# Performance work log

Measured on AMD Instinct MI355X. Metric: run time of the kernel, lower is better.

Reference implementation:

```python
import jax, jax.numpy as jnp
import numpy as np

B, L, HID, NH = 2, 2048, 1024, 16
HD = HID // NH  # 64


def setup_inputs() -> dict:
    key = jax.random.key(0)
    ks = jax.random.split(key, 12)
    s = 1.0 / np.sqrt(HID)
    query = jax.random.normal(ks[0], (B, L, HID), jnp.float32)
    key_t = jax.random.normal(ks[1], (B, L, HID), jnp.float32)
    value = jax.random.normal(ks[2], (B, L, HID), jnp.float32)
    # key padding mask: True = valid token; random lengths in [1024, 2048]
    lengths = jax.random.randint(ks[3], (B,), L // 2, L + 1)
    key_mask = jnp.arange(L)[None, :] < lengths[:, None]  # [B, K] bool
    # attn_mask: True = blocked (causal upper triangle), 2D branch [Q, K]
    attn_mask = jnp.triu(jnp.ones((L, L), jnp.bool_), k=1)
    Wq = jax.random.normal(ks[4], (HID, HID), jnp.float32) * s
    Wk = jax.random.normal(ks[5], (HID, HID), jnp.float32) * s
    Wv = jax.random.normal(ks[6], (HID, HID), jnp.float32) * s
    Wo = jax.random.normal(ks[7], (HID, HID), jnp.float32) * s
    bq = jax.random.normal(ks[8], (HID,), jnp.float32) * 0.01
    bk = jax.random.normal(ks[9], (HID,), jnp.float32) * 0.01
    bv = jax.random.normal(ks[10], (HID,), jnp.float32) * 0.01
    bo = jax.random.normal(ks[11], (HID,), jnp.float32) * 0.01
    return {"query": query, "key": key_t, "value": value,
            "key_mask": key_mask, "attn_mask": attn_mask,
            "Wq": Wq, "bq": bq, "Wk": Wk, "bk": bk,
            "Wv": Wv, "bv": bv, "Wo": Wo, "bo": bo}


def reference(query, key, value, key_mask, attn_mask,
              Wq, bq, Wk, bk, Wv, bv, Wo, bo):
    Bq, Q, _ = query.shape
    K = key.shape[1]
    # projections (torch Linear: x @ W.T + b), split heads -> [B, H, L, HD]
    def proj(x, W, b, L_):
        return (x @ W.T + b).reshape(Bq, L_, NH, HD).transpose(0, 2, 1, 3)
    q = proj(query, Wq, bq, Q)
    k = proj(key, Wk, bk, K)
    v = proj(value, Wv, bv, K)
    scores = jnp.einsum('bhqd,bhkd->bhqk', q, k) / np.sqrt(HD)
    blocked = attn_mask[None, None, :, :]                 # True = blocked
    kmask = key_mask[:, None, None, :]                    # True = valid
    valid = (~blocked) & kmask                            # [B,H,Q,K] (bcast)
    scores = jnp.where(blocked, -10000.0, scores)
    scores = jnp.where(kmask, scores, -10000.0)
    weights = jax.nn.softmax(scores, axis=-1)
    weights = weights * valid.astype(weights.dtype)
    weights = weights / jnp.maximum(weights.sum(-1, keepdims=True), 1e-6)
    attended = jnp.einsum('bhqk,bhkd->bhqd', weights, v)
    attended = attended.transpose(0, 2, 1, 3).reshape(Bq, Q, HID)
    return attended @ Wo.T + bo
```

## Files before the change

kernel.cpp:

```cpp
#include <hip/hip_runtime.h>
#include <hip/hip_bf16.h>
#include <stdint.h>


#define L_SEQ 2048
#define HID 1024
#define NHEAD 16
#define HD 64

typedef __attribute__((ext_vector_type(8))) short bf16x8;
typedef __attribute__((ext_vector_type(8))) unsigned short u16x8;
typedef __attribute__((ext_vector_type(4))) float f32x4;

__device__ __forceinline__ unsigned short f2bf(float f) {
  unsigned int u = __builtin_bit_cast(unsigned int, f);
  u += 0x7fffu + ((u >> 16) & 1u);
  return (unsigned short)(u >> 16);
}

__device__ __forceinline__ unsigned int pk2bf(float a, float b) {
  unsigned int r;
  asm("v_cvt_pk_bf16_f32 %0, %1, %2" : "=v"(r) : "v"(a), "v"(b));
  return r;
}

__device__ __forceinline__ void gl_lds16(const void* g, void* l) {
  __builtin_amdgcn_global_load_lds(
      (const __attribute__((address_space(1))) unsigned int*)(uintptr_t)g,
      (__attribute__((address_space(3))) unsigned int*)(uint32_t)(uintptr_t)l,
      16, 0, 0);
}

__device__ __forceinline__ f32x4 mfma16(bf16x8 a, bf16x8 b, f32x4 c) {
  return __builtin_amdgcn_mfma_f32_16x16x32_bf16(a, b, c, 0, 0, 0);
}

__global__ __launch_bounds__(256)
void convert_all_kernel(const float* __restrict__ q, const float* __restrict__ k,
                        const float* __restrict__ v, const float* __restrict__ wq,
                        const float* __restrict__ wk, const float* __restrict__ wv,
                        const float* __restrict__ wo, const unsigned int* __restrict__ km,
                        unsigned short* __restrict__ qb, unsigned short* __restrict__ kb,
                        unsigned short* __restrict__ vb, unsigned short* __restrict__ wqb,
                        unsigned short* __restrict__ wkb, unsigned short* __restrict__ wvb,
                        unsigned short* __restrict__ wob, int* __restrict__ lens) {
  __shared__ int red[256];
  const int bid = blockIdx.x;
  const int t = threadIdx.x;
  if (bid == 8192) {
    unsigned int w0 = km[0];
    bool u8mode = (w0 != 1u);
    for (int b = 0; b < 2; ++b) {
      int cnt = 0;
      if (u8mode) {
        const unsigned char* p = (const unsigned char*)km + b * L_SEQ;
        for (int i = t; i < L_SEQ; i += 256) cnt += (p[i] != 0) ? 1 : 0;
      } else {
        const unsigned int* p = km + b * L_SEQ;
        for (int i = t; i < L_SEQ; i += 256) cnt += (p[i] != 0) ? 1 : 0;
      }
      red[t] = cnt;
      __syncthreads();
      for (int s = 128; s > 0; s >>= 1) {
        if (t < s) red[t] += red[t + s];
        __syncthreads();
      }
      if (t == 0) lens[b] = red[0];
      __syncthreads();
    }
    return;
  }
  const float* src;
  unsigned short* dst;
  int base;
  if (bid < 6144) {
    int s = bid >> 11;
    base = (bid & 2047) * 2048;
    src = s == 0 ? q : (s == 1 ? k : v);
    dst = s == 0 ? qb : (s == 1 ? kb : vb);
  } else {
    int r = bid - 6144;
    int s = r >> 9;
    base = (r & 511) * 2048;
    src = s == 0 ? wq : (s == 1 ? wk : (s == 2 ? wv : wo));
    dst = s == 0 ? wqb : (s == 1 ? wkb : (s == 2 ? wvb : wob));
  }
  int i = base + t * 8;
  float4 a = *(const float4*)(src + i);
  float4 b4 = *(const float4*)(src + i + 4);
  u16x8 o;
  o[0] = f2bf(a.x); o[1] = f2bf(a.y); o[2] = f2bf(a.z); o[3] = f2bf(a.w);
  o[4] = f2bf(b4.x); o[5] = f2bf(b4.y); o[6] = f2bf(b4.z); o[7] = f2bf(b4.w);
  *(u16x8*)(dst + i) = o;
}

__device__ __forceinline__ void gemm128_core(const unsigned short* __restrict__ A,
                                             const unsigned short* __restrict__ W,
                                             int m0, int n0, int K,
                                             unsigned short* As, unsigned short* Bs,
                                             f32x4 acc[4][4]) {
  const int tid = threadIdx.x;
  const int w = tid >> 6, lane = tid & 63;
  const int l15 = lane & 15, l4 = lane >> 4;
  const int wr = w >> 1, wc = w & 1;
#pragma unroll
  for (int i = 0; i < 4; ++i)
#pragma unroll
    for (int j = 0; j < 4; ++j) acc[i][j] = (f32x4){0.f, 0.f, 0.f, 0.f};

  for (int k0 = 0; k0 < K; k0 += 32) {
#pragma unroll
    for (int i = 0; i < 2; ++i) {
      int c = i * 256 + tid;
      int row = c >> 2, col = (c & 3) * 8;
      gl_lds16(A + (size_t)(m0 + row) * K + k0 + col, (char*)As + (i * 256 + w * 64) * 16);
      gl_lds16(W + (size_t)(n0 + row) * K + k0 + col, (char*)Bs + (i * 256 + w * 64) * 16);
    }
    __syncthreads();
    bf16x8 af[4], bfr[4];
#pragma unroll
    for (int i = 0; i < 4; ++i)
      af[i] = *(const bf16x8*)(As + (wr * 64 + i * 16 + l15) * 32 + l4 * 8);
#pragma unroll
    for (int j = 0; j < 4; ++j)
      bfr[j] = *(const bf16x8*)(Bs + (wc * 64 + j * 16 + l15) * 32 + l4 * 8);
    __builtin_amdgcn_s_setprio(1);
#pragma unroll
    for (int i = 0; i < 4; ++i)
#pragma unroll
      for (int j = 0; j < 4; ++j) acc[i][j] = mfma16(af[i], bfr[j], acc[i][j]);
    __builtin_amdgcn_s_setprio(0);
    __syncthreads();
  }
}

__global__ __launch_bounds__(256)
void qkv_gemm_kernel(const unsigned short* __restrict__ qb, const unsigned short* __restrict__ kb,
                     const unsigned short* __restrict__ vb, const unsigned short* __restrict__ wq,
                     const unsigned short* __restrict__ wk, const unsigned short* __restrict__ wv,
                     const float* __restrict__ bq, const float* __restrict__ bk,
                     const float* __restrict__ bv, unsigned short* __restrict__ Qp,
                     unsigned short* __restrict__ Kp, unsigned short* __restrict__ Vtp) {
  __shared__ unsigned short As[128 * 32];
  __shared__ unsigned short Bs[128 * 32];
  const int z = blockIdx.z;
  const unsigned short* A = z == 0 ? qb : (z == 1 ? kb : vb);
  const unsigned short* W = z == 0 ? wq : (z == 1 ? wk : wv);
  const float* bias = z == 0 ? bq : (z == 1 ? bk : bv);
  const int m0 = blockIdx.y * 128, n0 = blockIdx.x * 128;
  f32x4 acc[4][4];
  gemm128_core(A, W, m0, n0, HID, As, Bs, acc);

  const int tid = threadIdx.x;
  const int w = tid >> 6, lane = tid & 63;
  const int l15 = lane & 15, l4 = lane >> 4;
  const int wr = w >> 1, wc = w & 1;
  const float scale = (z == 0) ? 0.125f * 1.44269504089f : 1.0f;
#pragma unroll
  for (int i = 0; i < 4; ++i)
#pragma unroll
    for (int j = 0; j < 4; ++j)
#pragma unroll
      for (int r = 0; r < 4; ++r) {
        int grow = m0 + wr * 64 + i * 16 + l4 * 4 + r;
        int gcol = n0 + wc * 64 + j * 16 + l15;
        float v = (acc[i][j][r] + bias[gcol]) * scale;
        int bb = grow >> 11, ll = grow & 2047;
        int hh = gcol >> 6, d = gcol & 63;
        unsigned short o = f2bf(v);
        if (z == 0)
          Qp[((size_t)(bb * NHEAD + hh) * L_SEQ + ll) * HD + d] = o;
        else if (z == 1)
          Kp[((size_t)(bb * NHEAD + hh) * L_SEQ + ll) * HD + d] = o;
        else
          Vtp[((size_t)(bb * NHEAD + hh) * HD + d) * L_SEQ + ll] = o;
      }
}

__global__ __launch_bounds__(256)
void out_gemm_kernel(const unsigned short* __restrict__ att, const unsigned short* __restrict__ wo,
                     const float* __restrict__ bo, float* __restrict__ out) {
  __shared__ unsigned short As[128 * 32];
  __shared__ unsigned short Bs[128 * 32];
  const int m0 = blockIdx.y * 128, n0 = blockIdx.x * 128;
  f32x4 acc[4][4];
  gemm128_core(att, wo, m0, n0, HID, As, Bs, acc);

  const int tid = threadIdx.x;
  const int w = tid >> 6, lane = tid & 63;
  const int l15 = lane & 15, l4 = lane >> 4;
  const int wr = w >> 1, wc = w & 1;
#pragma unroll
  for (int i = 0; i < 4; ++i)
#pragma unroll
    for (int j = 0; j < 4; ++j)
#pragma unroll
      for (int r = 0; r < 4; ++r) {
        int grow = m0 + wr * 64 + i * 16 + l4 * 4 + r;
        int gcol = n0 + wc * 64 + j * 16 + l15;
        out[(size_t)grow * HID + gcol] = acc[i][j][r] + bo[gcol];
      }
}

__global__ __launch_bounds__(512)
void attn_kernel(const unsigned short* __restrict__ Qp, const unsigned short* __restrict__ Kp,
                 const unsigned short* __restrict__ Vtp, unsigned short* __restrict__ att,
                 const int* __restrict__ lens) {
  __shared__ unsigned short Ks[2][64 * 64];
  __shared__ unsigned short Vs[2][64 * 64];
  __shared__ unsigned short Ps[8][16 * 72];

  const int x = blockIdx.x, bh = blockIdx.y;
  const int b = bh >> 4, h = bh & 15;
  const int tid = threadIdx.x, w = tid >> 6, lane = tid & 63;
  const int l15 = lane & 15, l4 = lane >> 4;
  const int len = lens[b];
  const int sub = (w < 4) ? x : (31 - x);
  const int qw0 = sub * 64 + (w & 3) * 16;

  const unsigned short* Qg = Qp + (size_t)bh * L_SEQ * HD;
  const unsigned short* Kg = Kp + (size_t)bh * L_SEQ * HD;
  const unsigned short* Vg = Vtp + (size_t)bh * HD * L_SEQ;

  const int rr = tid >> 3, cb = tid & 7;
  const int swz = (cb ^ (rr & 7)) * 8;
  const unsigned short* KgRow = Kg + (size_t)rr * HD + swz;
  const unsigned short* VgRow = Vg + (size_t)rr * L_SEQ + swz;

  bf16x8 qf[2];
#pragma unroll
  for (int kk = 0; kk < 2; ++kk)
    qf[kk] = *(const bf16x8*)(Qg + (size_t)(qw0 + l15) * HD + kk * 32 + l4 * 8);

  f32x4 acc[4];
#pragma unroll
  for (int n = 0; n < 4; ++n) acc[n] = (f32x4){0.f, 0.f, 0.f, 0.f};
  float mq = -1e30f, lq = 0.f;

  int koff[4][2];
#pragma unroll
  for (int n = 0; n < 4; ++n)
#pragma unroll
    for (int kk = 0; kk < 2; ++kk) {
      int row = n * 16 + l15;
      koff[n][kk] = row * 128 + (((l4 + kk * 4) ^ (row & 7)) * 16);
    }

  const int len_r = ((len + 63) >> 6) << 6;
  const int hi_end = 64 * (32 - x);
  const int kv_end = (hi_end < len_r) ? hi_end : len_r;
  const int nt = kv_end >> 6;

  gl_lds16(KgRow, (char*)&Ks[0][0] + w * 1024);
  gl_lds16(VgRow, (char*)&Vs[0][0] + w * 1024);
  __syncthreads();

  int cur = 0;
  for (int t = 0; t < nt; ++t) {
    const int k0 = t * 64;
    if (t + 1 < nt) {
      const int k1 = k0 + 64;
      gl_lds16(KgRow + (size_t)k1 * HD, (char*)&Ks[cur ^ 1][0] + w * 1024);
      gl_lds16(VgRow + k1, (char*)&Vs[cur ^ 1][0] + w * 1024);
    }
    if (k0 <= qw0 + 15) {
      const char* Kb = (const char*)&Ks[cur][0];
      const char* Vb = (const char*)&Vs[cur][0];
      f32x4 s[4];
#pragma unroll
      for (int n = 0; n < 4; ++n) s[n] = (f32x4){0.f, 0.f, 0.f, 0.f};
      __builtin_amdgcn_s_setprio(1);
#pragma unroll
      for (int kk = 0; kk < 2; ++kk) {
#pragma unroll
        for (int n = 0; n < 4; ++n)
          s[n] = mfma16(*(const bf16x8*)(Kb + koff[n][kk]), qf[kk], s[n]);
      }
      __builtin_amdgcn_s_setprio(0);
      if (!(k0 + 63 <= qw0 && k0 + 64 <= len)) {
        const int qa = qw0 + l15;
#pragma unroll
        for (int n = 0; n < 4; ++n)
#pragma unroll
          for (int r = 0; r < 4; ++r) {
            int ka = k0 + n * 16 + l4 * 4 + r;
            if (ka > qa || ka >= len) s[n][r] = -1e30f;
          }
      }
      float v01 = fmaxf(fmaxf(s[0][0], s[0][1]), fmaxf(s[0][2], s[0][3]));
      float v23 = fmaxf(fmaxf(s[1][0], s[1][1]), fmaxf(s[1][2], s[1][3]));
      float v45 = fmaxf(fmaxf(s[2][0], s[2][1]), fmaxf(s[2][2], s[2][3]));
      float v67 = fmaxf(fmaxf(s[3][0], s[3][1]), fmaxf(s[3][2], s[3][3]));
      float v = fmaxf(fmaxf(v01, v23), fmaxf(v45, v67));
      v = fmaxf(v, __shfl_xor(v, 16));
      v = fmaxf(v, __shfl_xor(v, 32));
      float mold = mq;
      float mnew = fmaxf(mold, v);
      mq = mnew;
      float alpha = __builtin_amdgcn_exp2f(mold - mnew);
      float rs = 0.f;
#pragma unroll
      for (int n = 0; n < 4; ++n)
#pragma unroll
        for (int r = 0; r < 4; ++r) {
          float p = __builtin_amdgcn_exp2f(s[n][r] - mnew);
          s[n][r] = p;
          rs += p;
        }
      rs += __shfl_xor(rs, 16);
      rs += __shfl_xor(rs, 32);
      lq = lq * alpha + rs;
      float ar[4];
#pragma unroll
      for (int r = 0; r < 4; ++r) ar[r] = __shfl(alpha, l4 * 4 + r, 64);
#pragma unroll
      for (int n = 0; n < 4; ++n)
#pragma unroll
        for (int r = 0; r < 4; ++r) acc[n][r] *= ar[r];
#pragma unroll
      for (int n = 0; n < 4; ++n) {
        uint2 pw;
        pw.x = pk2bf(s[n][0], s[n][1]);
        pw.y = pk2bf(s[n][2], s[n][3]);
        *(uint2*)(&Ps[w][l15 * 72 + n * 16 + l4 * 4]) = pw;
      }
      bf16x8 pf[2];
#pragma unroll
      for (int kk = 0; kk < 2; ++kk)
        pf[kk] = *(const bf16x8*)(&Ps[w][l15 * 72 + kk * 32 + l4 * 8]);
      __builtin_amdgcn_s_setprio(1);
#pragma unroll
      for (int kk = 0; kk < 2; ++kk) {
#pragma unroll
        for (int n = 0; n < 4; ++n)
          acc[n] = mfma16(pf[kk], *(const bf16x8*)(Vb + koff[n][kk]), acc[n]);
      }
      __builtin_amdgcn_s_setprio(0);
    }
    __syncthreads();
    cur ^= 1;
  }

  float invq = 1.0f / lq;
  float invr[4];
#pragma unroll
  for (int r = 0; r < 4; ++r) invr[r] = __shfl(invq, l4 * 4 + r, 64);
#pragma unroll
  for (int r = 0; r < 4; ++r) {
    int qa = qw0 + l4 * 4 + r;
#pragma unroll
    for (int n = 0; n < 4; ++n)
      att[((size_t)(b * L_SEQ + qa)) * HID + h * HD + n * 16 + l15] = f2bf(acc[n][r] * invr[r]);
  }
}

extern "C" void kernel_launch(void* const* d_in, const int* in_sizes, int n_in,
                              void* d_out, int out_size, void* d_ws, size_t ws_size,
                              hipStream_t stream) {
  const float* query = (const float*)d_in[0];
  const float* key = (const float*)d_in[1];
  const float* value = (const float*)d_in[2];
  const unsigned int* key_mask = (const unsigned int*)d_in[3];
  const float* Wq = (const float*)d_in[5];
  const float* bq = (const float*)d_in[6];
  const float* Wk = (const float*)d_in[7];
  const float* bk = (const float*)d_in[8];
  const float* Wv = (const float*)d_in[9];
  const float* bv = (const float*)d_in[10];
  const float* Wo = (const float*)d_in[11];
  const float* bo = (const float*)d_in[12];

  char* ws = (char*)d_ws;
  const size_t SZ_X = (size_t)4096 * 1024 * 2;
  const size_t SZ_W = (size_t)1024 * 1024 * 2;
  unsigned short* qb = (unsigned short*)(ws);
  unsigned short* kb = (unsigned short*)(ws + SZ_X);
  unsigned short* vb = (unsigned short*)(ws + 2 * SZ_X);
  unsigned short* wqb = (unsigned short*)(ws + 3 * SZ_X);
  unsigned short* wkb = (unsigned short*)(ws + 3 * SZ_X + SZ_W);
  unsigned short* wvb = (unsigned short*)(ws + 3 * SZ_X + 2 * SZ_W);
  unsigned short* wob = (unsigned short*)(ws + 3 * SZ_X + 3 * SZ_W);
  unsigned short* Qp = (unsigned short*)(ws + 3 * SZ_X + 4 * SZ_W);
  unsigned short* Kp = (unsigned short*)(ws + 4 * SZ_X + 4 * SZ_W);
  unsigned short* Vtp = (unsigned short*)(ws + 5 * SZ_X + 4 * SZ_W);
  unsigned short* att = (unsigned short*)(ws + 6 * SZ_X + 4 * SZ_W);
  int* lens = (int*)(ws + 7 * SZ_X + 4 * SZ_W);

  convert_all_kernel<<<8193, 256, 0, stream>>>(query, key, value, Wq, Wk, Wv, Wo, key_mask,
                                               qb, kb, vb, wqb, wkb, wvb, wob, lens);
  qkv_gemm_kernel<<<dim3(8, 32, 3), 256, 0, stream>>>(qb, kb, vb, wqb, wkb, wvb, bq, bk, bv,
                                                      Qp, Kp, Vtp);
  attn_kernel<<<dim3(16, 32), 512, 0, stream>>>(Qp, Kp, Vtp, att, lens);
  out_gemm_kernel<<<dim3(8, 32), 256, 0, stream>>>(att, wob, bo, (float*)d_out);
}
```

Baseline: 146.8 us.

## Double-buffer GEMM LDS tiles, vectorize V-transpose stores, lazy softmax rescale

The shared 128x128 GEMM core now double-buffers its LDS tiles, so the next K-slice's global-to-LDS load is issued before the current slice's MFMAs and one barrier per iteration is removed. The QKV epilogue for V writes four consecutive sequence positions as one packed 8-byte store into the transposed layout instead of scalar 2-byte stores. The attention kernel skips the running-max update and accumulator rescale unless some lane's new max exceeds the old one by more than 8 (in log2 units). This lets unnormalized probabilities grow up to 2^8 before rescaling, and it doubles LDS use per GEMM block, which may lower occupancy.

New measurement: 129.7 us. 11.6% less time.

```diff
diff --git a/kernel.cpp b/kernel.cpp
--- a/kernel.cpp
+++ b/kernel.cpp
@@ -94,11 +94,11 @@
   *(u16x8*)(dst + i) = o;
 }
 
-__device__ __forceinline__ void gemm128_core(const unsigned short* __restrict__ A,
-                                             const unsigned short* __restrict__ W,
-                                             int m0, int n0, int K,
-                                             unsigned short* As, unsigned short* Bs,
-                                             f32x4 acc[4][4]) {
+__device__ __forceinline__ void gemm128_bf_core(const unsigned short* __restrict__ A,
+                                                const unsigned short* __restrict__ W,
+                                                int m0, int n0, int K,
+                                                unsigned short* As, unsigned short* Bs,
+                                                f32x4 acc[4][4]) {
   const int tid = threadIdx.x;
   const int w = tid >> 6, lane = tid & 63;
   const int l15 = lane & 15, l4 = lane >> 4;
@@ -108,22 +108,39 @@
 #pragma unroll
     for (int j = 0; j < 4; ++j) acc[i][j] = (f32x4){0.f, 0.f, 0.f, 0.f};
 
-  for (int k0 = 0; k0 < K; k0 += 32) {
-#pragma unroll
-    for (int i = 0; i < 2; ++i) {
-      int c = i * 256 + tid;
-      int row = c >> 2, col = (c & 3) * 8;
-      gl_lds16(A + (size_t)(m0 + row) * K + k0 + col, (char*)As + (i * 256 + w * 64) * 16);
-      gl_lds16(W + (size_t)(n0 + row) * K + k0 + col, (char*)Bs + (i * 256 + w * 64) * 16);
+  const int nk = K >> 5;
+#pragma unroll
+  for (int i = 0; i < 2; ++i) {
+    int c = i * 256 + tid;
+    int row = c >> 2, col = (c & 3) * 8;
+    gl_lds16(A + (size_t)(m0 + row) * K + col, (char*)As + (i * 256 + w * 64) * 16);
+    gl_lds16(W + (size_t)(n0 + row) * K + col, (char*)Bs + (i * 256 + w * 64) * 16);
+  }
+  __syncthreads();
+
+  int cur = 0;
+  for (int t = 0; t < nk; ++t) {
+    const int k0 = t * 32;
+    if (t + 1 < nk) {
+#pragma unroll
+      for (int i = 0; i < 2; ++i) {
+        int c = i * 256 + tid;
+        int row = c >> 2, col = (c & 3) * 8;
+        gl_lds16(A + (size_t)(m0 + row) * K + k0 + 32 + col,
+                 (char*)As + (cur ^ 1) * 8192 + (i * 256 + w * 64) * 16);
+        gl_lds16(W + (size_t)(n0 + row) * K + k0 + 32 + col,
+                 (char*)Bs + (cur ^ 1) * 8192 + (i * 256 + w * 64) * 16);
+      }
     }
-    __syncthreads();
+    const unsigned short* Asb = As + cur * 4096;
+    const unsigned short* Bsb = Bs + cur * 4096;
     bf16x8 af[4], bfr[4];
 #pragma unroll
     for (int i = 0; i < 4; ++i)
-      af[i] = *(const bf16x8*)(As + (wr * 64 + i * 16 + l15) * 32 + l4 * 8);
+      af[i] = *(const bf16x8*)(Asb + (wr * 64 + i * 16 + l15) * 32 + l4 * 8);
 #pragma unroll
     for (int j = 0; j < 4; ++j)
-      bfr[j] = *(const bf16x8*)(Bs + (wc * 64 + j * 16 + l15) * 32 + l4 * 8);
+      bfr[j] = *(const bf16x8*)(Bsb + (wc * 64 + j * 16 + l15) * 32 + l4 * 8);
     __builtin_amdgcn_s_setprio(1);
 #pragma unroll
     for (int i = 0; i < 4; ++i)
@@ -131,6 +148,7 @@
       for (int j = 0; j < 4; ++j) acc[i][j] = mfma16(af[i], bfr[j], acc[i][j]);
     __builtin_amdgcn_s_setprio(0);
     __syncthreads();
+    cur ^= 1;
   }
 }
 
@@ -141,50 +159,62 @@
                      const float* __restrict__ bq, const float* __restrict__ bk,
                      const float* __restrict__ bv, unsigned short* __restrict__ Qp,
                      unsigned short* __restrict__ Kp, unsigned short* __restrict__ Vtp) {
-  __shared__ unsigned short As[128 * 32];
-  __shared__ unsigned short Bs[128 * 32];
+  __shared__ unsigned short As[2 * 128 * 32];
+  __shared__ unsigned short Bs[2 * 128 * 32];
   const int z = blockIdx.z;
   const unsigned short* A = z == 0 ? qb : (z == 1 ? kb : vb);
   const unsigned short* W = z == 0 ? wq : (z == 1 ? wk : wv);
   const float* bias = z == 0 ? bq : (z == 1 ? bk : bv);
   const int m0 = blockIdx.y * 128, n0 = blockIdx.x * 128;
   f32x4 acc[4][4];
-  gemm128_core(A, W, m0, n0, HID, As, Bs, acc);
+  gemm128_bf_core(A, W, m0, n0, HID, As, Bs, acc);
 
   const int tid = threadIdx.x;
   const int w = tid >> 6, lane = tid & 63;
   const int l15 = lane & 15, l4 = lane >> 4;
   const int wr = w >> 1, wc = w & 1;
   const float scale = (z == 0) ? 0.125f * 1.44269504089f : 1.0f;
-#pragma unroll
-  for (int i = 0; i < 4; ++i)
-#pragma unroll
-    for (int j = 0; j < 4; ++j)
-#pragma unroll
-      for (int r = 0; r < 4; ++r) {
-        int grow = m0 + wr * 64 + i * 16 + l4 * 4 + r;
+  if (z == 2) {
+#pragma unroll
+    for (int i = 0; i < 4; ++i)
+#pragma unroll
+      for (int j = 0; j < 4; ++j) {
+        int grow0 = m0 + wr * 64 + i * 16 + l4 * 4;
         int gcol = n0 + wc * 64 + j * 16 + l15;
-        float v = (acc[i][j][r] + bias[gcol]) * scale;
-        int bb = grow >> 11, ll = grow & 2047;
+        float bv_ = bias[gcol];
+        int bb = grow0 >> 11, ll0 = grow0 & 2047;
         int hh = gcol >> 6, d = gcol & 63;
-        unsigned short o = f2bf(v);
-        if (z == 0)
-          Qp[((size_t)(bb * NHEAD + hh) * L_SEQ + ll) * HD + d] = o;
-        else if (z == 1)
-          Kp[((size_t)(bb * NHEAD + hh) * L_SEQ + ll) * HD + d] = o;
-        else
-          Vtp[((size_t)(bb * NHEAD + hh) * HD + d) * L_SEQ + ll] = o;
-      }
+        uint2 pw;
+        pw.x = pk2bf(acc[i][j][0] + bv_, acc[i][j][1] + bv_);
+        pw.y = pk2bf(acc[i][j][2] + bv_, acc[i][j][3] + bv_);
+        *(uint2*)(&Vtp[((size_t)(bb * NHEAD + hh) * HD + d) * L_SEQ + ll0]) = pw;
+      }
+  } else {
+    unsigned short* P = (z == 0) ? Qp : Kp;
+#pragma unroll
+    for (int i = 0; i < 4; ++i)
+#pragma unroll
+      for (int j = 0; j < 4; ++j)
+#pragma unroll
+        for (int r = 0; r < 4; ++r) {
+          int grow = m0 + wr * 64 + i * 16 + l4 * 4 + r;
+          int gcol = n0 + wc * 64 + j * 16 + l15;
+          float v = (acc[i][j][r] + bias[gcol]) * scale;
+          int bb = grow >> 11, ll = grow & 2047;
+          int hh = gcol >> 6, d = gcol & 63;
+          P[((size_t)(bb * NHEAD + hh) * L_SEQ + ll) * HD + d] = f2bf(v);
+        }
+  }
 }
 
 __global__ __launch_bounds__(256)
 void out_gemm_kernel(const unsigned short* __restrict__ att, const unsigned short* __restrict__ wo,
                      const float* __restrict__ bo, float* __restrict__ out) {
-  __shared__ unsigned short As[128 * 32];
-  __shared__ unsigned short Bs[128 * 32];
+  __shared__ unsigned short As[2 * 128 * 32];
+  __shared__ unsigned short Bs[2 * 128 * 32];
   const int m0 = blockIdx.y * 128, n0 = blockIdx.x * 128;
   f32x4 acc[4][4];
-  gemm128_core(att, wo, m0, n0, HID, As, Bs, acc);
+  gemm128_bf_core(att, wo, m0, n0, HID, As, Bs, acc);
 
   const int tid = threadIdx.x;
   const int w = tid >> 6, lane = tid & 63;
@@ -294,29 +324,31 @@
       float v = fmaxf(fmaxf(v01, v23), fmaxf(v45, v67));
       v = fmaxf(v, __shfl_xor(v, 16));
       v = fmaxf(v, __shfl_xor(v, 32));
-      float mold = mq;
-      float mnew = fmaxf(mold, v);
-      mq = mnew;
-      float alpha = __builtin_amdgcn_exp2f(mold - mnew);
+      if (!__all(v - mq <= 8.0f)) {
+        float mnew = fmaxf(mq, v);
+        float alpha = __builtin_amdgcn_exp2f(mq - mnew);
+        mq = mnew;
+        float ar[4];
+#pragma unroll
+        for (int r = 0; r < 4; ++r) ar[r] = __shfl(alpha, l4 * 4 + r, 64);
+#pragma unroll
+        for (int n = 0; n < 4; ++n)
+#pragma unroll
+          for (int r = 0; r < 4; ++r) acc[n][r] *= ar[r];
+        lq *= alpha;
+      }
       float rs = 0.f;
 #pragma unroll
       for (int n = 0; n < 4; ++n)
 #pragma unroll
         for (int r = 0; r < 4; ++r) {
-          float p = __builtin_amdgcn_exp2f(s[n][r] - mnew);
+          float p = __builtin_amdgcn_exp2f(s[n][r] - mq);
           s[n][r] = p;
           rs += p;
         }
       rs += __shfl_xor(rs, 16);
       rs += __shfl_xor(rs, 32);
-      lq = lq * alpha + rs;
-      float ar[4];
-#pragma unroll
-      for (int r = 0; r < 4; ++r) ar[r] = __shfl(alpha, l4 * 4 + r, 64);
-#pragma unroll
-      for (int n = 0; n < 4; ++n)
-#pragma unroll
-        for (int r = 0; r < 4; ++r) acc[n][r] *= ar[r];
+      lq += rs;
 #pragma unroll
       for (int n = 0; n < 4; ++n) {
         uint2 pw;
```
